# Optimization experiments

Hardware: AMD Instinct MI355X
Metric: run time of the kernel (lower is better)

## Reference

```python
import jax, jax.numpy as jnp
import numpy as np

B, S, D, EXP = 2, 2048, 128, 16
N = D * EXP  # state_dim = 2048


def setup_inputs() -> dict:
    key = jax.random.key(0)
    ks = jax.random.split(key, 11)
    s_in = 1.0 / np.sqrt(D)   # torch Linear default init bound for dim->N layers
    s_out = 1.0 / np.sqrt(N)  # for out_proj (N->dim)
    x = jax.random.normal(ks[0], (B, S, D), dtype=jnp.float32)
    W_B = jax.random.uniform(ks[1], (N, D), jnp.float32, -s_in, s_in)
    b_B = jax.random.uniform(ks[2], (N,), jnp.float32, -s_in, s_in)
    W_C = jax.random.uniform(ks[3], (N, D), jnp.float32, -s_in, s_in)
    b_C = jax.random.uniform(ks[4], (N,), jnp.float32, -s_in, s_in)
    W_dt = jax.random.uniform(ks[5], (N, D), jnp.float32, -s_in, s_in)
    b_dt = jax.random.uniform(ks[6], (N,), jnp.float32, -s_in, s_in)
    A_log = jnp.log(jax.random.uniform(ks[7], (N,), jnp.float32) * 0.5 + 0.5)
    W_out = jax.random.uniform(ks[8], (D, N), jnp.float32, -s_out, s_out)
    b_out = jax.random.uniform(ks[9], (D,), jnp.float32, -s_out, s_out)
    return {"x": x, "W_B": W_B, "b_B": b_B, "W_C": W_C, "b_C": b_C,
            "W_dt": W_dt, "b_dt": b_dt, "A_log": A_log,
            "W_out": W_out, "b_out": b_out}


def reference(x, W_B, b_B, W_C, b_C, W_dt, b_dt, A_log, W_out, b_out):
    # Featurizer projections: [B,S,D] -> [B,S,N]
    B_feat = jnp.einsum('bsd,nd->bsn', x, W_B) + b_B
    C_feat = jnp.einsum('bsd,nd->bsn', x, W_C) + b_C
    dt = jax.nn.softplus(jnp.einsum('bsd,nd->bsn', x, W_dt) + b_dt)
    A = -jnp.exp(A_log)                # [N]
    A_bar = jnp.exp(dt * A)            # [B,S,N]
    B_bar = dt * B_feat                # [B,S,N]

    # Sequential diagonal scan: h_t = A_t * h_{t-1} + B_t ; y_t = C_t * h_t
    def step(h, abc):
        a_t, b_t, c_t = abc            # each [B,N]
        h = a_t * h + b_t
        return h, c_t * h

    h0 = jnp.zeros((x.shape[0], N), dtype=x.dtype)
    xs = (jnp.swapaxes(A_bar, 0, 1),   # [S,B,N]
          jnp.swapaxes(B_bar, 0, 1),
          jnp.swapaxes(C_feat, 0, 1))
    _, ys = jax.lax.scan(step, h0, xs)  # ys: [S,B,N]
    y = jnp.swapaxes(ys, 0, 1)          # [B,S,N]
    return jnp.einsum('bsn,dn->bsd', y, W_out) + b_out
```

## Files before the change

### kernel.cpp

```cpp
#include <hip/hip_runtime.h>


#define BB 2
#define SS 2048
#define DDIM 128
#define NDIM 2048
#define TT (BB*SS)
#define NTILE (TT/16)

typedef short short8 __attribute__((ext_vector_type(8)));
typedef float floatx4 __attribute__((ext_vector_type(4)));

__device__ __forceinline__ unsigned short f2b(float f){
  unsigned u = __float_as_uint(f);
  u += 0x7FFFu + ((u >> 16) & 1u);
  return (unsigned short)(u >> 16);
}
__device__ __forceinline__ float softplus_f(float v){
  return v > 15.f ? v : __logf(1.f + __expf(v));
}
__device__ __forceinline__ void pack8(const float* __restrict__ s,
                                      unsigned short* __restrict__ d){
  floatx4 v0 = *(const floatx4*)s;
  floatx4 v1 = *(const floatx4*)(s + 4);
  short8 r;
  r[0]=(short)f2b(v0[0]); r[1]=(short)f2b(v0[1]); r[2]=(short)f2b(v0[2]); r[3]=(short)f2b(v0[3]);
  r[4]=(short)f2b(v1[0]); r[5]=(short)f2b(v1[1]); r[6]=(short)f2b(v1[2]); r[7]=(short)f2b(v1[3]);
  *(short8*)d = r;
}

__global__ void prep_kernel(const float* __restrict__ x,
                            const float* __restrict__ W_B,
                            const float* __restrict__ W_C,
                            const float* __restrict__ W_dt,
                            const float* __restrict__ A_log,
                            const float* __restrict__ W_out,
                            unsigned short* __restrict__ xp,
                            unsigned short* __restrict__ Wp3,
                            unsigned short* __restrict__ Wop,
                            float* __restrict__ Aval,
                            unsigned long long* __restrict__ Sbuf){
  const int gid = blockIdx.x * blockDim.x + threadIdx.x;
  if (gid < 32768) Sbuf[gid] = 0ull;
  if (gid < 2048) Aval[gid] = -__expf(A_log[gid]);
  if (gid < 65536){
    int g = gid, tile = g >> 8, kk = (g >> 6) & 3, lane = g & 63;
    int q = lane >> 4, m = lane & 15;
    pack8(x + (size_t)(tile*16 + m)*DDIM + kk*32 + q*8, xp + (size_t)g*8);
  }
  if (gid < 98304){
    int mat = gid >> 15, g = gid & 32767;
    const float* W = (mat == 0) ? W_B : (mat == 1 ? W_dt : W_C);
    int tile = g >> 8, kk = (g >> 6) & 3, lane = g & 63;
    int q = lane >> 4, m = lane & 15;
    pack8(W + (size_t)(tile*16 + m)*DDIM + kk*32 + q*8,
          Wp3 + (size_t)mat*262144 + (size_t)g*8);
  }
  if (gid < 32768){
    int g = gid, tile = g >> 12, kk = (g >> 6) & 63, lane = g & 63;
    int q = lane >> 4, m = lane & 15;
    pack8(W_out + (size_t)(tile*16 + m)*NDIM + kk*32 + q*8, Wop + (size_t)g*8);
  }
}

__global__ __launch_bounds__(256, 2) void projscan_kernel(
    const unsigned short* __restrict__ xp,
    const unsigned short* __restrict__ Wp3,
    const float* __restrict__ b_B,
    const float* __restrict__ b_dt,
    const float* __restrict__ b_C,
    const float* __restrict__ Aval,
    unsigned long long* __restrict__ Sbuf,
    unsigned short* __restrict__ ybp){
  __shared__ unsigned short sW[3*4096];
  __shared__ unsigned short sYT[4][16*40];
  __shared__ float sPw[4][32], sHw[4][32];
  __shared__ float sIw[4][32];
  const int tid  = threadIdx.x;
  const int lane = tid & 63;
  const int wv   = tid >> 6;
  const int m    = lane & 15;
  const int q    = lane >> 4;
  const int bx   = blockIdx.x;
  const int by   = blockIdx.y;
  const int n0   = by*32;

  for (int i = tid; i < 1536; i += 256){
    int mat = i >> 9, rem = i & 511;
    *(short8*)(sW + mat*4096 + rem*8) =
        *(const short8*)(Wp3 + (size_t)mat*262144 + (size_t)by*4096 + rem*8);
  }
  __syncthreads();

  float bBv[2], bDv[2], bCv[2], Avv[2];
#pragma unroll
  for (int nt = 0; nt < 2; ++nt){
    const int n = n0 + nt*16 + m;
    bBv[nt] = b_B[n]; bDv[nt] = b_dt[n]; bCv[nt] = b_C[n]; Avv[nt] = Aval[n];
  }

  unsigned ypk[4][2][2], cpk[4][2][2];
  float pe_t[4][2], he_t[4][2];
  float pa_run[2] = {1.f, 1.f}, ha_run[2] = {0.f, 0.f};

#pragma unroll
  for (int i = 0; i < 4; ++i){
    const int tile = bx*16 + wv*4 + i;
    short8 xf[4];
#pragma unroll
    for (int kk = 0; kk < 4; ++kk)
      xf[kk] = *(const short8*)(xp + (size_t)tile*2048 + kk*512 + lane*8);

    floatx4 acc[3][2];
#pragma unroll
    for (int mat = 0; mat < 3; ++mat)
#pragma unroll
      for (int nt = 0; nt < 2; ++nt)
        acc[mat][nt] = (floatx4){0.f,0.f,0.f,0.f};
#pragma unroll
    for (int nt = 0; nt < 2; ++nt)
#pragma unroll
      for (int kk = 0; kk < 4; ++kk){
        short8 wB = *(const short8*)(sW +         nt*2048 + kk*512 + lane*8);
        short8 wD = *(const short8*)(sW + 4096 +  nt*2048 + kk*512 + lane*8);
        short8 wC = *(const short8*)(sW + 8192 +  nt*2048 + kk*512 + lane*8);
        acc[0][nt] = __builtin_amdgcn_mfma_f32_16x16x32_bf16(xf[kk], wB, acc[0][nt], 0, 0, 0);
        acc[1][nt] = __builtin_amdgcn_mfma_f32_16x16x32_bf16(xf[kk], wD, acc[1][nt], 0, 0, 0);
        acc[2][nt] = __builtin_amdgcn_mfma_f32_16x16x32_bf16(xf[kk], wC, acc[2][nt], 0, 0, 0);
      }

#pragma unroll
    for (int nt = 0; nt < 2; ++nt){
      float Ar[4], Br[4], Cc[4];
#pragma unroll
      for (int r = 0; r < 4; ++r){
        float dtv = softplus_f(acc[1][nt][r] + bDv[nt]);
        Ar[r] = __expf(dtv * Avv[nt]);
        Br[r] = dtv * (acc[0][nt][r] + bBv[nt]);
        Cc[r] = acc[2][nt][r] + bCv[nt];
      }
      float P = Ar[0], H = Br[0];
#pragma unroll
      for (int r = 1; r < 4; ++r){ H = Ar[r]*H + Br[r]; P *= Ar[r]; }
      float pp = __shfl(P, (lane - 16) & 63, 64);
      float hh = __shfl(H, (lane - 16) & 63, 64);
      if (q >= 1){ H = P*hh + H; P *= pp; }
      pp = __shfl(P, (lane - 32) & 63, 64);
      hh = __shfl(H, (lane - 32) & 63, 64);
      if (q >= 2){ H = P*hh + H; P *= pp; }
      float pe = __shfl(P, (lane - 16) & 63, 64);
      float he = __shfl(H, (lane - 16) & 63, 64);
      if (q == 0){ pe = 1.f; he = 0.f; }
      float pb = __shfl(P, m + 48, 64);
      float hb = __shfl(H, m + 48, 64);

      float h = he, pa = pe;
      unsigned short yr[4], cr[4];
#pragma unroll
      for (int r = 0; r < 4; ++r){
        h = Ar[r]*h + Br[r];
        pa *= Ar[r];
        yr[r] = f2b(Cc[r]*h);
        cr[r] = f2b(Cc[r]*pa);
      }
      ypk[i][nt][0] = (unsigned)yr[0] | ((unsigned)yr[1] << 16);
      ypk[i][nt][1] = (unsigned)yr[2] | ((unsigned)yr[3] << 16);
      cpk[i][nt][0] = (unsigned)cr[0] | ((unsigned)cr[1] << 16);
      cpk[i][nt][1] = (unsigned)cr[2] | ((unsigned)cr[3] << 16);

      pe_t[i][nt] = pa_run[nt];
      he_t[i][nt] = ha_run[nt];
      ha_run[nt] = pb*ha_run[nt] + hb;
      pa_run[nt] *= pb;
    }
  }
  if (q == 0){
#pragma unroll
    for (int nt = 0; nt < 2; ++nt){
      sPw[wv][nt*16 + m] = pa_run[nt];
      sHw[wv][nt*16 + m] = ha_run[nt];
    }
  }
  __syncthreads();

  if (tid < 32){
    float Pw[4], Hw[4];
#pragma unroll
    for (int w2 = 0; w2 < 4; ++w2){ Pw[w2] = sPw[w2][tid]; Hw[w2] = sHw[w2][tid]; }
    float Sj = 0.f;
    if (bx & 7){
      unsigned long long* src = Sbuf + (size_t)(by*16 + bx - 1)*32 + tid;
      unsigned long long v;
      for (;;){
        v = __hip_atomic_load(src, __ATOMIC_RELAXED, __HIP_MEMORY_SCOPE_AGENT);
        if ((unsigned)(v >> 32) == 1u) break;
        __builtin_amdgcn_s_sleep(2);
      }
      Sj = __uint_as_float((unsigned)v);
    }
    float s = Sj;
#pragma unroll
    for (int w2 = 0; w2 < 4; ++w2){
      sIw[w2][tid] = s;
      s = Pw[w2]*s + Hw[w2];
    }
    unsigned long long pv = (1ull << 32) | (unsigned long long)__float_as_uint(s);
    __hip_atomic_store(Sbuf + (size_t)(by*16 + bx)*32 + tid, pv,
                       __ATOMIC_RELAXED, __HIP_MEMORY_SCOPE_AGENT);
  }
  __syncthreads();

  float iw[2];
#pragma unroll
  for (int nt = 0; nt < 2; ++nt) iw[nt] = sIw[wv][nt*16 + m];
#pragma unroll
  for (int i = 0; i < 4; ++i){
    const int tile = bx*16 + wv*4 + i;
#pragma unroll
    for (int nt = 0; nt < 2; ++nt){
      float it = pe_t[i][nt]*iw[nt] + he_t[i][nt];
#pragma unroll
      for (int j = 0; j < 2; ++j){
        unsigned yp = ypk[i][nt][j], cp = cpk[i][nt][j];
        float y0 = __uint_as_float(yp << 16);
        float y1 = __uint_as_float(yp & 0xffff0000u);
        float c0 = __uint_as_float(cp << 16);
        float c1 = __uint_as_float(cp & 0xffff0000u);
        sYT[wv][(q*4 + j*2 + 0)*40 + nt*16 + m] = f2b(y0 + c0*it);
        sYT[wv][(q*4 + j*2 + 1)*40 + nt*16 + m] = f2b(y1 + c1*it);
      }
    }
    short8 yv = *(const short8*)&sYT[wv][m*40 + q*8];
    *(short8*)(ybp + (size_t)tile*32768 + (size_t)by*512 + (size_t)lane*8) = yv;
  }
}

__global__ void outproj_kernel(const unsigned short* __restrict__ ybp,
                               const unsigned short* __restrict__ Wop,
                               const float* __restrict__ b_out,
                               float* __restrict__ out){
  __shared__ float red[4*2048];
  const int tid  = threadIdx.x;
  const int lane = tid & 63;
  const int wv   = tid >> 6;
  const int m    = lane & 15;
  const int q    = lane >> 4;
  const int tile = blockIdx.x;

  floatx4 acc[8];
#pragma unroll
  for (int dt = 0; dt < 8; ++dt) acc[dt] = (floatx4){0.f,0.f,0.f,0.f};

  const unsigned short* aP = ybp + (size_t)tile*32768 + lane*8;
  const unsigned short* bP = Wop + (size_t)lane*8;
#pragma unroll 4
  for (int kk = wv*16; kk < wv*16 + 16; ++kk){
    short8 af = *(const short8*)(aP + (size_t)kk*512);
#pragma unroll
    for (int dt = 0; dt < 8; ++dt){
      short8 bf = *(const short8*)(bP + (size_t)dt*32768 + (size_t)kk*512);
      acc[dt] = __builtin_amdgcn_mfma_f32_16x16x32_bf16(af, bf, acc[dt], 0, 0, 0);
    }
  }
#pragma unroll
  for (int dt = 0; dt < 8; ++dt)
#pragma unroll
    for (int r = 0; r < 4; ++r)
      red[wv*2048 + (q*4 + r)*128 + dt*16 + m] = acc[dt][r];
  __syncthreads();
#pragma unroll
  for (int i = 0; i < 8; ++i){
    int idx = i*256 + tid;
    float s = red[idx] + red[2048 + idx] + red[4096 + idx] + red[6144 + idx];
    int tl = idx >> 7, d = idx & 127;
    out[(size_t)(tile*16 + tl)*DDIM + d] = s + b_out[d];
  }
}

extern "C" void kernel_launch(void* const* d_in, const int* in_sizes, int n_in,
                              void* d_out, int out_size, void* d_ws, size_t ws_size,
                              hipStream_t stream) {
  const float* x     = (const float*)d_in[0];
  const float* W_B   = (const float*)d_in[1];
  const float* b_B   = (const float*)d_in[2];
  const float* W_C   = (const float*)d_in[3];
  const float* b_C   = (const float*)d_in[4];
  const float* W_dt  = (const float*)d_in[5];
  const float* b_dt  = (const float*)d_in[6];
  const float* A_log = (const float*)d_in[7];
  const float* W_out = (const float*)d_in[8];
  const float* b_out = (const float*)d_in[9];
  float* out = (float*)d_out;

  char* w = (char*)d_ws;
  unsigned short* xp    = (unsigned short*)(w + 0x0000000);
  unsigned short* Wp3   = (unsigned short*)(w + 0x0100000);
  unsigned short* Wop   = (unsigned short*)(w + 0x0280000);
  float*          Aval  = (float*)         (w + 0x0300000);
  unsigned short* ybp   = (unsigned short*)(w + 0x0310000);
  unsigned long long* Sbuf = (unsigned long long*)(w + 0x1310000);

  prep_kernel<<<384, 256, 0, stream>>>(
      x, W_B, W_C, W_dt, A_log, W_out, xp, Wp3, Wop, Aval, Sbuf);

  projscan_kernel<<<dim3(16, 64), 256, 0, stream>>>(
      xp, Wp3, b_B, b_dt, b_C, Aval, Sbuf, ybp);

  outproj_kernel<<<NTILE, 256, 0, stream>>>(ybp, Wop, b_out, out);
}
```

Measured before the change: 119.6 us.

## Replace serial carry chain with decoupled lookback over block-local aggregates

Each block now publishes its own local (product, hidden) aggregate right away instead of waiting for the previous block's inclusive prefix. A block then polls all earlier blocks in its 8-block segment and composes their aggregates itself, so the serial dependency chain across blocks goes away. This costs twice the scratch buffer, more polling loads and some redundant composition work in each block.

```diff
diff --git a/kernel.cpp b/kernel.cpp
--- a/kernel.cpp
+++ b/kernel.cpp
@@ -41,7 +41,7 @@
                             float* __restrict__ Aval,
                             unsigned long long* __restrict__ Sbuf){
   const int gid = blockIdx.x * blockDim.x + threadIdx.x;
-  if (gid < 32768) Sbuf[gid] = 0ull;
+  if (gid < 65536) Sbuf[gid] = 0ull;
   if (gid < 2048) Aval[gid] = -__expf(A_log[gid]);
   if (gid < 65536){
     int g = gid, tile = g >> 8, kk = (g >> 6) & 3, lane = g & 63;
@@ -187,26 +187,54 @@
     float Pw[4], Hw[4];
 #pragma unroll
     for (int w2 = 0; w2 < 4; ++w2){ Pw[w2] = sPw[w2][tid]; Hw[w2] = sHw[w2][tid]; }
-    float Sj = 0.f;
-    if (bx & 7){
-      unsigned long long* src = Sbuf + (size_t)(by*16 + bx - 1)*32 + tid;
-      unsigned long long v;
+    float pb = 1.f, hb = 0.f;
+#pragma unroll
+    for (int w2 = 0; w2 < 4; ++w2){ hb = Pw[w2]*hb + Hw[w2]; pb *= Pw[w2]; }
+    unsigned long long* dst = Sbuf + ((size_t)(by*16 + bx)*32 + tid)*2;
+    __hip_atomic_store(dst,   (1ull << 32) | (unsigned long long)__float_as_uint(pb),
+                       __ATOMIC_RELAXED, __HIP_MEMORY_SCOPE_AGENT);
+    __hip_atomic_store(dst+1, (1ull << 32) | (unsigned long long)__float_as_uint(hb),
+                       __ATOMIC_RELAXED, __HIP_MEMORY_SCOPE_AGENT);
+    float S = 0.f;
+    const int cnt = bx & 7;
+    if (cnt){
+      const int j0 = bx & ~7;
+      unsigned long long vp0=0,vp1=0,vp2=0,vp3=0,vp4=0,vp5=0,vp6=0;
+      unsigned long long vh0=0,vh1=0,vh2=0,vh3=0,vh4=0,vh5=0,vh6=0;
+      unsigned got = 0;
+      const unsigned all = (1u << cnt) - 1u;
+      const unsigned long long* base = Sbuf + ((size_t)(by*16 + j0)*32 + tid)*2;
       for (;;){
-        v = __hip_atomic_load(src, __ATOMIC_RELAXED, __HIP_MEMORY_SCOPE_AGENT);
-        if ((unsigned)(v >> 32) == 1u) break;
-        __builtin_amdgcn_s_sleep(2);
-      }
-      Sj = __uint_as_float((unsigned)v);
-    }
-    float s = Sj;
+#define LOOKBACK(J, VP, VH)                                                     \
+        if (J < cnt && !(got & (1u << J))){                                     \
+          unsigned long long a = __hip_atomic_load(base + (size_t)J*64,         \
+              __ATOMIC_RELAXED, __HIP_MEMORY_SCOPE_AGENT);                      \
+          unsigned long long b = __hip_atomic_load(base + (size_t)J*64 + 1,     \
+              __ATOMIC_RELAXED, __HIP_MEMORY_SCOPE_AGENT);                      \
+          if (((unsigned)(a >> 32) & (unsigned)(b >> 32)) == 1u){               \
+            VP = a; VH = b; got |= 1u << J;                                     \
+          }                                                                     \
+        }
+        LOOKBACK(0, vp0, vh0) LOOKBACK(1, vp1, vh1) LOOKBACK(2, vp2, vh2)
+        LOOKBACK(3, vp3, vh3) LOOKBACK(4, vp4, vh4) LOOKBACK(5, vp5, vh5)
+        LOOKBACK(6, vp6, vh6)
+#undef LOOKBACK
+        if (got == all) break;
+        __builtin_amdgcn_s_sleep(1);
+      }
+#define COMPOSE(J, VP, VH)                                                      \
+      if (J < cnt) S = __uint_as_float((unsigned)VP)*S + __uint_as_float((unsigned)VH);
+      COMPOSE(0, vp0, vh0) COMPOSE(1, vp1, vh1) COMPOSE(2, vp2, vh2)
+      COMPOSE(3, vp3, vh3) COMPOSE(4, vp4, vh4) COMPOSE(5, vp5, vh5)
+      COMPOSE(6, vp6, vh6)
+#undef COMPOSE
+    }
+    float s = S;
 #pragma unroll
     for (int w2 = 0; w2 < 4; ++w2){
       sIw[w2][tid] = s;
       s = Pw[w2]*s + Hw[w2];
     }
-    unsigned long long pv = (1ull << 32) | (unsigned long long)__float_as_uint(s);
-    __hip_atomic_store(Sbuf + (size_t)(by*16 + bx)*32 + tid, pv,
-                       __ATOMIC_RELAXED, __HIP_MEMORY_SCOPE_AGENT);
   }
   __syncthreads();
 
```

New measurement: 117.6 us. About the same (-1.6%).
